# Kernel tuning notes

Measured on AMD Instinct MI355X. Metric: run time of the kernel, lower is better.

## Reference

```python
import jax, jax.numpy as jnp
import numpy as np


def setup_inputs() -> dict:
    key = jax.random.key(0)
    k1, k2 = jax.random.split(key)
    B, H, W, C_IN, N_SUMS = 32, 128, 128, 32, 32
    # x holds log-probabilities coming from a previous SPN layer
    x = jax.random.normal(k1, (B, H, W, C_IN), dtype=jnp.float32)
    # logspace accumulators (raw logits; normalized via log_softmax over axis=2)
    accumulators = jax.random.normal(k2, (1, 1, C_IN, N_SUMS), dtype=jnp.float32)
    return {"x": x, "accumulators": accumulators}


def reference(x, accumulators):
    # log_softmax over the input-channel axis (axis=2 of [1,1,Cin,S])
    log_w = jax.nn.log_softmax(accumulators, axis=2)[0, 0]  # [Cin, S]
    # logconv1x1_2d: out[b,h,w,s] = logsumexp_c( x[b,h,w,c] + log_w[c,s] )
    # Implemented as a stable log-matmul to avoid materializing [B,H,W,C,S].
    m = jnp.max(x, axis=-1, keepdims=True)              # [B,H,W,1]
    p = jnp.exp(x - m)                                   # [B,H,W,Cin]
    w = jnp.exp(log_w)                                   # [Cin,S], entries <= 1
    out = m + jnp.log(jnp.einsum("bhwc,cs->bhws", p, w))  # [B,H,W,S]
    return out
```

## Files before the change

kernel.cpp:

```cpp
#include <hip/hip_runtime.h>
#include <hip/hip_bf16.h>
#include <math.h>

constexpr int CIN = 32;
constexpr int NS  = 32;

typedef __attribute__((ext_vector_type(8)))  short  short8;
typedef __attribute__((ext_vector_type(16))) float  f32x16;

__device__ __forceinline__ short f2bf(float f) {
    union { float f; unsigned u; } v; v.f = f;
    unsigned r = (v.u + 0x7FFFu + ((v.u >> 16) & 1u)) >> 16;
    return (short)r;
}

__device__ __forceinline__ unsigned pk2bf(float lo, float hi) {
    union { __hip_bfloat162 b; unsigned u; } cv;
    cv.b = __float22bfloat162_rn(float2{lo, hi});
    return cv.u;
}

__global__ __launch_bounds__(256)
void logconv_fused(const float* __restrict__ x,
                   const float* __restrict__ acc,
                   float* __restrict__ out) {
    __shared__ short8 wfrag[64][2];

    const int lane = threadIdx.x & 63;
    const int wid  = threadIdx.x >> 6;
    const int r    = lane & 31;
    const int h    = lane >> 5;
    const long pixA = (long)blockIdx.x * 256 + wid * 64 + r;
    const long pixB = pixA + 32;

    const float* xpA = x + pixA * CIN + 8 * h;
    float4 a0 = *(const float4*)(xpA);
    float4 a1 = *(const float4*)(xpA + 4);
    float4 a2 = *(const float4*)(xpA + 16);
    float4 a3 = *(const float4*)(xpA + 20);
    const float* xpB = x + pixB * CIN + 8 * h;
    float4 b0 = *(const float4*)(xpB);
    float4 b1 = *(const float4*)(xpB + 4);
    float4 b2 = *(const float4*)(xpB + 16);
    float4 b3 = *(const float4*)(xpB + 20);

    if (threadIdx.x < 32) {
        const int s = threadIdx.x;
        float a[CIN];
#pragma unroll
        for (int c = 0; c < CIN; ++c) a[c] = acc[c * NS + s];
        float wm = a[0];
#pragma unroll
        for (int c = 1; c < CIN; ++c) wm = fmaxf(wm, a[c]);
        float wsum = 0.f;
#pragma unroll
        for (int c = 0; c < CIN; ++c) { a[c] = __expf(a[c] - wm); wsum += a[c]; }
        float winv = 1.f / wsum;
        short8 f00, f01, f10, f11;
#pragma unroll
        for (int j = 0; j < 8; ++j) {
            f00[j] = f2bf(a[j]      * winv);
            f10[j] = f2bf(a[8 + j]  * winv);
            f01[j] = f2bf(a[16 + j] * winv);
            f11[j] = f2bf(a[24 + j] * winv);
        }
        wfrag[s][0]      = f00;
        wfrag[s][1]      = f01;
        wfrag[32 + s][0] = f10;
        wfrag[32 + s][1] = f11;
    }
    __syncthreads();

    const short8 w0 = wfrag[lane][0];
    const short8 w1 = wfrag[lane][1];

#define COMPUTE(PIX, R0, R1, R2, R3) do {                               \
        union { short8 s; unsigned u[4]; } pu0, pu1;                    \
        pu0.u[0] = pk2bf(__expf(R0.x), __expf(R0.y));                   \
        pu0.u[1] = pk2bf(__expf(R0.z), __expf(R0.w));                   \
        pu0.u[2] = pk2bf(__expf(R1.x), __expf(R1.y));                   \
        pu0.u[3] = pk2bf(__expf(R1.z), __expf(R1.w));                   \
        pu1.u[0] = pk2bf(__expf(R2.x), __expf(R2.y));                   \
        pu1.u[1] = pk2bf(__expf(R2.z), __expf(R2.w));                   \
        pu1.u[2] = pk2bf(__expf(R3.x), __expf(R3.y));                   \
        pu1.u[3] = pk2bf(__expf(R3.z), __expf(R3.w));                   \
        f32x16 accv;                                                    \
        _Pragma("unroll")                                               \
        for (int i = 0; i < 16; ++i) accv[i] = 0.f;                     \
        accv = __builtin_amdgcn_mfma_f32_32x32x16_bf16(w0, pu0.s, accv, 0, 0, 0); \
        accv = __builtin_amdgcn_mfma_f32_32x32x16_bf16(w1, pu1.s, accv, 0, 0, 0); \
        float* op_ = out + (PIX) * NS;                                  \
        _Pragma("unroll")                                               \
        for (int g = 0; g < 4; ++g) {                                   \
            float4 v;                                                   \
            v.x = __logf(accv[4 * g + 0]);                              \
            v.y = __logf(accv[4 * g + 1]);                              \
            v.z = __logf(accv[4 * g + 2]);                              \
            v.w = __logf(accv[4 * g + 3]);                              \
            *(float4*)(op_ + 8 * g + 4 * h) = v;                        \
        }                                                               \
    } while (0)

    COMPUTE(pixA, a0, a1, a2, a3);
    COMPUTE(pixB, b0, b1, b2, b3);
#undef COMPUTE
}

extern "C" void kernel_launch(void* const* d_in, const int* in_sizes, int n_in,
                              void* d_out, int out_size, void* d_ws, size_t ws_size,
                              hipStream_t stream) {
    const float* x   = (const float*)d_in[0];
    const float* acc = (const float*)d_in[1];
    float* out = (float*)d_out;

    int npix = in_sizes[0] / CIN;
    int grid = npix / 256;
    logconv_fused<<<grid, 256, 0, stream>>>(x, acc, out);
}
```

Before: 28.32 us.

## Software-pipeline four pixel tiles per wave with inline-asm loads and stores

Each wave now handles four 32-pixel tiles instead of two, and the grid shrinks to match. Loads for the next tile are issued with inline-asm global_load_dwordx4 before the current tile's exp/MFMA/log work, with explicit s_waitcnt vmcnt counts and sched barriers to double-buffer registers. Outputs go through inline-asm global stores. The goal is to overlap memory latency with compute and to spread the per-block softmax weight setup over more pixels. The cost is fragile manual waitcnt accounting and fewer blocks in flight.

```diff
diff --git a/kernel.cpp b/kernel.cpp
--- a/kernel.cpp
+++ b/kernel.cpp
@@ -5,6 +5,7 @@
 constexpr int CIN = 32;
 constexpr int NS  = 32;
 
+typedef __attribute__((ext_vector_type(4)))  float  f32x4;
 typedef __attribute__((ext_vector_type(8)))  short  short8;
 typedef __attribute__((ext_vector_type(16))) float  f32x16;
 
@@ -21,28 +22,33 @@
 }
 
 __global__ __launch_bounds__(256)
-void logconv_fused(const float* __restrict__ x,
-                   const float* __restrict__ acc,
-                   float* __restrict__ out) {
+void logconv_pipe(const float* __restrict__ x,
+                  const float* __restrict__ acc,
+                  float* __restrict__ out) {
     __shared__ short8 wfrag[64][2];
 
     const int lane = threadIdx.x & 63;
     const int wid  = threadIdx.x >> 6;
     const int r    = lane & 31;
     const int h    = lane >> 5;
-    const long pixA = (long)blockIdx.x * 256 + wid * 64 + r;
-    const long pixB = pixA + 32;
 
-    const float* xpA = x + pixA * CIN + 8 * h;
-    float4 a0 = *(const float4*)(xpA);
-    float4 a1 = *(const float4*)(xpA + 4);
-    float4 a2 = *(const float4*)(xpA + 16);
-    float4 a3 = *(const float4*)(xpA + 20);
-    const float* xpB = x + pixB * CIN + 8 * h;
-    float4 b0 = *(const float4*)(xpB);
-    float4 b1 = *(const float4*)(xpB + 4);
-    float4 b2 = *(const float4*)(xpB + 16);
-    float4 b3 = *(const float4*)(xpB + 20);
+    const long tile0 = ((long)blockIdx.x * 4 + wid) * 4;
+    const long pix0  = tile0 * 32 + r;
+
+    const float* xp0 = x + pix0 * CIN + 8 * h;
+    const float* xp1 = xp0 + 32 * CIN;
+    const float* xp2 = xp1 + 32 * CIN;
+    const float* xp3 = xp2 + 32 * CIN;
+
+#define LOADT(XP, R0, R1, R2, R3) do {                                      \
+        asm volatile("global_load_dwordx4 %0, %1, off"            : "=v"(R0) : "v"(XP)); \
+        asm volatile("global_load_dwordx4 %0, %1, off offset:16"  : "=v"(R1) : "v"(XP)); \
+        asm volatile("global_load_dwordx4 %0, %1, off offset:64"  : "=v"(R2) : "v"(XP)); \
+        asm volatile("global_load_dwordx4 %0, %1, off offset:80"  : "=v"(R3) : "v"(XP)); \
+    } while (0)
+
+    f32x4 c0, c1, c2, c3, n0, n1, n2, n3;
+    LOADT(xp0, c0, c1, c2, c3);
 
     if (threadIdx.x < 32) {
         const int s = threadIdx.x;
@@ -74,7 +80,7 @@
     const short8 w0 = wfrag[lane][0];
     const short8 w1 = wfrag[lane][1];
 
-#define COMPUTE(PIX, R0, R1, R2, R3) do {                               \
+#define COMPUTE_STORE(T, R0, R1, R2, R3) do {                           \
         union { short8 s; unsigned u[4]; } pu0, pu1;                    \
         pu0.u[0] = pk2bf(__expf(R0.x), __expf(R0.y));                   \
         pu0.u[1] = pk2bf(__expf(R0.z), __expf(R0.w));                   \
@@ -89,21 +95,40 @@
         for (int i = 0; i < 16; ++i) accv[i] = 0.f;                     \
         accv = __builtin_amdgcn_mfma_f32_32x32x16_bf16(w0, pu0.s, accv, 0, 0, 0); \
         accv = __builtin_amdgcn_mfma_f32_32x32x16_bf16(w1, pu1.s, accv, 0, 0, 0); \
-        float* op_ = out + (PIX) * NS;                                  \
-        _Pragma("unroll")                                               \
-        for (int g = 0; g < 4; ++g) {                                   \
-            float4 v;                                                   \
-            v.x = __logf(accv[4 * g + 0]);                              \
-            v.y = __logf(accv[4 * g + 1]);                              \
-            v.z = __logf(accv[4 * g + 2]);                              \
-            v.w = __logf(accv[4 * g + 3]);                              \
-            *(float4*)(op_ + 8 * g + 4 * h) = v;                        \
-        }                                                               \
+        float* op_ = out + (pix0 + (T) * 32) * NS + 4 * h;              \
+        f32x4 v0, v1, v2, v3;                                           \
+        v0.x = __logf(accv[0]);  v0.y = __logf(accv[1]);                \
+        v0.z = __logf(accv[2]);  v0.w = __logf(accv[3]);                \
+        v1.x = __logf(accv[4]);  v1.y = __logf(accv[5]);                \
+        v1.z = __logf(accv[6]);  v1.w = __logf(accv[7]);                \
+        v2.x = __logf(accv[8]);  v2.y = __logf(accv[9]);                \
+        v2.z = __logf(accv[10]); v2.w = __logf(accv[11]);               \
+        v3.x = __logf(accv[12]); v3.y = __logf(accv[13]);               \
+        v3.z = __logf(accv[14]); v3.w = __logf(accv[15]);               \
+        asm volatile("global_store_dwordx4 %0, %1, off"           :: "v"(op_), "v"(v0)); \
+        asm volatile("global_store_dwordx4 %0, %1, off offset:32" :: "v"(op_), "v"(v1)); \
+        asm volatile("global_store_dwordx4 %0, %1, off offset:64" :: "v"(op_), "v"(v2)); \
+        asm volatile("global_store_dwordx4 %0, %1, off offset:96" :: "v"(op_), "v"(v3)); \
     } while (0)
 
-    COMPUTE(pixA, a0, a1, a2, a3);
-    COMPUTE(pixB, b0, b1, b2, b3);
-#undef COMPUTE
+    LOADT(xp1, n0, n1, n2, n3);
+    asm volatile("s_waitcnt vmcnt(4)");
+    __builtin_amdgcn_sched_barrier(0);
+    COMPUTE_STORE(0, c0, c1, c2, c3);
+    LOADT(xp2, c0, c1, c2, c3);
+    asm volatile("s_waitcnt vmcnt(8)");
+    __builtin_amdgcn_sched_barrier(0);
+    COMPUTE_STORE(1, n0, n1, n2, n3);
+    LOADT(xp3, n0, n1, n2, n3);
+    asm volatile("s_waitcnt vmcnt(8)");
+    __builtin_amdgcn_sched_barrier(0);
+    COMPUTE_STORE(2, c0, c1, c2, c3);
+    asm volatile("s_waitcnt vmcnt(4)");
+    __builtin_amdgcn_sched_barrier(0);
+    COMPUTE_STORE(3, n0, n1, n2, n3);
+
+#undef LOADT
+#undef COMPUTE_STORE
 }
 
 extern "C" void kernel_launch(void* const* d_in, const int* in_sizes, int n_in,
@@ -114,6 +139,6 @@
     float* out = (float*)d_out;
 
     int npix = in_sizes[0] / CIN;
-    int grid = npix / 256;
-    logconv_fused<<<grid, 256, 0, stream>>>(x, acc, out);
+    int grid = npix / (4 * 4 * 32);
+    logconv_pipe<<<grid, 256, 0, stream>>>(x, acc, out);
 }
```

Measured after the change: 27.60 us. 2.5% less time.

## Stage input and output tiles through swizzled LDS for fully coalesced global traffic

Applied to the files above, without the earlier changes.

Each wave now processes four 32-pixel tiles. Inputs are loaded asynchronously into double-buffered LDS with global_load_lds and an XOR swizzle, and the loads of later tiles overlap the compute of earlier ones. The log results are written back into LDS and then stored with contiguous per-lane 16-byte writes, replacing the old strided per-pixel accesses. The grid is reduced fourfold. This trades more LDS traffic, manual vmcnt waits and fewer blocks for coalescing and overlap.

```diff
diff --git a/kernel.cpp b/kernel.cpp
--- a/kernel.cpp
+++ b/kernel.cpp
@@ -5,8 +5,12 @@
 constexpr int CIN = 32;
 constexpr int NS  = 32;
 
+typedef __attribute__((ext_vector_type(4)))  float  f32x4;
 typedef __attribute__((ext_vector_type(8)))  short  short8;
 typedef __attribute__((ext_vector_type(16))) float  f32x16;
+
+typedef __attribute__((address_space(1))) unsigned int gbl_u32;
+typedef __attribute__((address_space(3))) unsigned int lds_u32;
 
 __device__ __forceinline__ short f2bf(float f) {
     union { float f; unsigned u; } v; v.f = f;
@@ -21,28 +25,41 @@
 }
 
 __global__ __launch_bounds__(256)
-void logconv_fused(const float* __restrict__ x,
-                   const float* __restrict__ acc,
-                   float* __restrict__ out) {
+void logconv_coal(const float* __restrict__ x,
+                  const float* __restrict__ acc,
+                  float* __restrict__ out) {
     __shared__ short8 wfrag[64][2];
+    __shared__ __align__(16) char bufs[4][2][4096];
 
     const int lane = threadIdx.x & 63;
     const int wid  = threadIdx.x >> 6;
     const int r    = lane & 31;
     const int h    = lane >> 5;
-    const long pixA = (long)blockIdx.x * 256 + wid * 64 + r;
-    const long pixB = pixA + 32;
+    const int swz  = (lane * 16) ^ ((lane >> 3) << 4);
+    const int rx   = (r & 7) << 4;
 
-    const float* xpA = x + pixA * CIN + 8 * h;
-    float4 a0 = *(const float4*)(xpA);
-    float4 a1 = *(const float4*)(xpA + 4);
-    float4 a2 = *(const float4*)(xpA + 16);
-    float4 a3 = *(const float4*)(xpA + 20);
-    const float* xpB = x + pixB * CIN + 8 * h;
-    float4 b0 = *(const float4*)(xpB);
-    float4 b1 = *(const float4*)(xpB + 4);
-    float4 b2 = *(const float4*)(xpB + 16);
-    float4 b3 = *(const float4*)(xpB + 20);
+    const long tile0 = ((long)blockIdx.x * 4 + wid) * 4;
+    const char* xbase = (const char*)x + tile0 * 4096;
+    char*       obase = (char*)out      + tile0 * 4096;
+
+#define GLD(T, BUF) do {                                                    \
+        const char* s_ = xbase + (size_t)(T) * 4096;                        \
+        char* l_ = (char*)&bufs[wid][BUF][0];                               \
+        _Pragma("unroll")                                                   \
+        for (int k_ = 0; k_ < 4; ++k_) {                                    \
+            __builtin_amdgcn_global_load_lds(                               \
+                (const gbl_u32*)(s_ + k_ * 1024 + swz),                     \
+                (lds_u32*)(l_ + k_ * 1024), 16, 0, 0);                      \
+        }                                                                   \
+    } while (0)
+
+#define VMWAIT(N) do {                                                     \
+        asm volatile("s_waitcnt vmcnt(" #N ")" ::: "memory");               \
+        __builtin_amdgcn_sched_barrier(0);                                  \
+    } while (0)
+
+    GLD(0, 0);
+    GLD(1, 1);
 
     if (threadIdx.x < 32) {
         const int s = threadIdx.x;
@@ -74,36 +91,66 @@
     const short8 w0 = wfrag[lane][0];
     const short8 w1 = wfrag[lane][1];
 
-#define COMPUTE(PIX, R0, R1, R2, R3) do {                               \
-        union { short8 s; unsigned u[4]; } pu0, pu1;                    \
-        pu0.u[0] = pk2bf(__expf(R0.x), __expf(R0.y));                   \
-        pu0.u[1] = pk2bf(__expf(R0.z), __expf(R0.w));                   \
-        pu0.u[2] = pk2bf(__expf(R1.x), __expf(R1.y));                   \
-        pu0.u[3] = pk2bf(__expf(R1.z), __expf(R1.w));                   \
-        pu1.u[0] = pk2bf(__expf(R2.x), __expf(R2.y));                   \
-        pu1.u[1] = pk2bf(__expf(R2.z), __expf(R2.w));                   \
-        pu1.u[2] = pk2bf(__expf(R3.x), __expf(R3.y));                   \
-        pu1.u[3] = pk2bf(__expf(R3.z), __expf(R3.w));                   \
-        f32x16 accv;                                                    \
-        _Pragma("unroll")                                               \
-        for (int i = 0; i < 16; ++i) accv[i] = 0.f;                     \
+#define TILE(T, BUF) do {                                                   \
+        char* b_ = (char*)&bufs[wid][BUF][0];                               \
+        const f32x4 xa = *(const f32x4*)(b_ + r * 128 + ((32 * h)      ^ rx)); \
+        const f32x4 xb = *(const f32x4*)(b_ + r * 128 + ((32 * h + 16) ^ rx)); \
+        const f32x4 xc = *(const f32x4*)(b_ + r * 128 + ((64 + 32 * h) ^ rx)); \
+        const f32x4 xd = *(const f32x4*)(b_ + r * 128 + ((80 + 32 * h) ^ rx)); \
+        union { short8 s; unsigned u[4]; } pu0, pu1;                        \
+        pu0.u[0] = pk2bf(__expf(xa.x), __expf(xa.y));                       \
+        pu0.u[1] = pk2bf(__expf(xa.z), __expf(xa.w));                       \
+        pu0.u[2] = pk2bf(__expf(xb.x), __expf(xb.y));                       \
+        pu0.u[3] = pk2bf(__expf(xb.z), __expf(xb.w));                       \
+        pu1.u[0] = pk2bf(__expf(xc.x), __expf(xc.y));                       \
+        pu1.u[1] = pk2bf(__expf(xc.z), __expf(xc.w));                       \
+        pu1.u[2] = pk2bf(__expf(xd.x), __expf(xd.y));                       \
+        pu1.u[3] = pk2bf(__expf(xd.z), __expf(xd.w));                       \
+        f32x16 accv;                                                        \
+        _Pragma("unroll")                                                   \
+        for (int i = 0; i < 16; ++i) accv[i] = 0.f;                         \
         accv = __builtin_amdgcn_mfma_f32_32x32x16_bf16(w0, pu0.s, accv, 0, 0, 0); \
         accv = __builtin_amdgcn_mfma_f32_32x32x16_bf16(w1, pu1.s, accv, 0, 0, 0); \
-        float* op_ = out + (PIX) * NS;                                  \
-        _Pragma("unroll")                                               \
-        for (int g = 0; g < 4; ++g) {                                   \
-            float4 v;                                                   \
-            v.x = __logf(accv[4 * g + 0]);                              \
-            v.y = __logf(accv[4 * g + 1]);                              \
-            v.z = __logf(accv[4 * g + 2]);                              \
-            v.w = __logf(accv[4 * g + 3]);                              \
-            *(float4*)(op_ + 8 * g + 4 * h) = v;                        \
-        }                                                               \
+        f32x4 v0, v1, v2, v3;                                               \
+        v0.x = __logf(accv[0]);  v0.y = __logf(accv[1]);                    \
+        v0.z = __logf(accv[2]);  v0.w = __logf(accv[3]);                    \
+        v1.x = __logf(accv[4]);  v1.y = __logf(accv[5]);                    \
+        v1.z = __logf(accv[6]);  v1.w = __logf(accv[7]);                    \
+        v2.x = __logf(accv[8]);  v2.y = __logf(accv[9]);                    \
+        v2.z = __logf(accv[10]); v2.w = __logf(accv[11]);                   \
+        v3.x = __logf(accv[12]); v3.y = __logf(accv[13]);                   \
+        v3.z = __logf(accv[14]); v3.w = __logf(accv[15]);                   \
+         \
+          \
+        *(f32x4*)(b_ + r * 128 + ((  0 + 16 * h) ^ rx)) = v0;               \
+        *(f32x4*)(b_ + r * 128 + (( 32 + 16 * h) ^ rx)) = v1;               \
+        *(f32x4*)(b_ + r * 128 + (( 64 + 16 * h) ^ rx)) = v2;               \
+        *(f32x4*)(b_ + r * 128 + (( 96 + 16 * h) ^ rx)) = v3;               \
+        asm volatile("" ::: "memory");   \
+        const f32x4 o0 = *(const f32x4*)(b_ +    0 + swz);                  \
+        const f32x4 o1 = *(const f32x4*)(b_ + 1024 + swz);                  \
+        const f32x4 o2 = *(const f32x4*)(b_ + 2048 + swz);                  \
+        const f32x4 o3 = *(const f32x4*)(b_ + 3072 + swz);                  \
+        char* op_ = obase + (size_t)(T) * 4096 + lane * 16;                 \
+        *(f32x4*)(op_ +    0) = o0;                                         \
+        *(f32x4*)(op_ + 1024) = o1;                                         \
+        *(f32x4*)(op_ + 2048) = o2;                                         \
+        *(f32x4*)(op_ + 3072) = o3;                                         \
     } while (0)
 
-    COMPUTE(pixA, a0, a1, a2, a3);
-    COMPUTE(pixB, b0, b1, b2, b3);
-#undef COMPUTE
+    TILE(0, 0);
+    GLD(2, 0);
+    VMWAIT(8);
+    TILE(1, 1);
+    GLD(3, 1);
+    VMWAIT(8);
+    TILE(2, 0);
+    VMWAIT(4);
+    TILE(3, 1);
+
+#undef GLD
+#undef VMWAIT
+#undef TILE
 }
 
 extern "C" void kernel_launch(void* const* d_in, const int* in_sizes, int n_in,
@@ -114,6 +161,6 @@
     float* out = (float*)d_out;
 
     int npix = in_sizes[0] / CIN;
-    int grid = npix / 256;
-    logconv_fused<<<grid, 256, 0, stream>>>(x, acc, out);
+    int grid = npix / (4 * 4 * 32);
+    logconv_coal<<<grid, 256, 0, stream>>>(x, acc, out);
 }
```

After: 25.94 us. 1.09x faster.
